# Performance work log

Hardware: AMD Instinct MI355X
Metric: run time of the kernel (lower is better)

## Reference

```python
import jax, jax.numpy as jnp
from jax import lax
import numpy as np

D, H, L, B, T = 64, 16, 8, 4096, 128

def _uniform(key, shape, k):
    return jax.random.uniform(key, shape, jnp.float32, -k, k)

def setup_inputs() -> dict:
    key = jax.random.key(0)
    ks = jax.random.split(key, 16)
    kh = 1.0 / np.sqrt(H)
    kl = 1.0 / np.sqrt(L)
    return {
        "x": jax.random.normal(ks[0], (B, T, D), jnp.float32),
        # encoder LSTM (PyTorch gate order i,f,g,o stacked along dim 0)
        "enc_Wih": _uniform(ks[1], (4 * H, D), kh),
        "enc_Whh": _uniform(ks[2], (4 * H, H), kh),
        "enc_bih": _uniform(ks[3], (4 * H,), kh),
        "enc_bhh": _uniform(ks[4], (4 * H,), kh),
        # to_latent / from_latent linears
        "Wl": _uniform(ks[5], (L, H), kh),
        "bl": _uniform(ks[6], (L,), kh),
        "Wf": _uniform(ks[7], (H, L), kl),
        "bf": _uniform(ks[8], (H,), kl),
        # decoder LSTM (input size H)
        "dec_Wih": _uniform(ks[9], (4 * H, H), kh),
        "dec_Whh": _uniform(ks[10], (4 * H, H), kh),
        "dec_bih": _uniform(ks[11], (4 * H,), kh),
        "dec_bhh": _uniform(ks[12], (4 * H,), kh),
        # output linear H -> D
        "Wo": _uniform(ks[13], (D, H), kh),
        "bo": _uniform(ks[14], (D,), kh),
    }

def _lstm(x_tbd, Wih, Whh, bih, bhh):
    # x_tbd: [T, B, in]; returns (all hidden [T, B, H], final hidden [B, H])
    b = bih + bhh
    nbatch = x_tbd.shape[1]
    h0 = jnp.zeros((nbatch, H), x_tbd.dtype)
    c0 = jnp.zeros((nbatch, H), x_tbd.dtype)
    # precompute input projections for all timesteps (one big GEMM)
    xg = jnp.einsum('tbd,gd->tbg', x_tbd, Wih) + b  # [T, B, 4H]
    def step(carry, xg_t):
        h, c = carry
        gates = xg_t + h @ Whh.T
        i, f, g, o = jnp.split(gates, 4, axis=-1)
        c = jax.nn.sigmoid(f) * c + jax.nn.sigmoid(i) * jnp.tanh(g)
        h = jax.nn.sigmoid(o) * jnp.tanh(c)
        return (h, c), h
    (hT, _), hs = lax.scan(step, (h0, c0), xg)
    return hs, hT

def reference(x, enc_Wih, enc_Whh, enc_bih, enc_bhh, Wl, bl, Wf, bf,
              dec_Wih, dec_Whh, dec_bih, dec_bhh, Wo, bo):
    seq = x.shape[1]
    x_t = jnp.swapaxes(x, 0, 1)  # [T, B, D]
    _, h_enc = _lstm(x_t, enc_Wih, enc_Whh, enc_bih, enc_bhh)  # [B, H]
    latent = h_enc @ Wl.T + bl                                  # [B, L]
    rep = latent @ Wf.T + bf                                    # [B, H]
    rep_t = jnp.broadcast_to(rep[None], (seq,) + rep.shape)     # [T, B, H]
    hs, _ = _lstm(rep_t, dec_Wih, dec_Whh, dec_bih, dec_bhh)    # [T, B, H]
    out = jnp.einsum('tbh,dh->tbd', hs, Wo) + bo                # [T, B, D]
    return jnp.swapaxes(out, 0, 1)                              # [B, T, D]
```

## Files before the change

kernel.cpp:

```cpp
#include <hip/hip_runtime.h>
#include <stdint.h>


constexpr int Dm = 64, Tm = 128, TB = 16;

typedef __bf16 bf16x8 __attribute__((ext_vector_type(8)));
typedef float f32x4 __attribute__((ext_vector_type(4)));
typedef unsigned int u32x4 __attribute__((ext_vector_type(4)));

__device__ __forceinline__ uint32_t pk_hi(float a, float b) {
  return (__float_as_uint(b) & 0xFFFF0000u) | (__float_as_uint(a) >> 16);
}
__device__ __forceinline__ float trunc_bf(float a) {
  return __uint_as_float(__float_as_uint(a) & 0xFFFF0000u);
}
__device__ __forceinline__ f32x4 mfma16(bf16x8 a, bf16x8 b, f32x4 c) {
  return __builtin_amdgcn_mfma_f32_16x16x32_bf16(a, b, c, 0, 0, 0);
}

__device__ __forceinline__ float fexp2(float x) {
#if __has_builtin(__builtin_amdgcn_exp2f)
  return __builtin_amdgcn_exp2f(x);
#else
  return exp2f(x);
#endif
}
__device__ __forceinline__ float frcp(float x) {
#if __has_builtin(__builtin_amdgcn_rcpf)
  return __builtin_amdgcn_rcpf(x);
#else
  return 1.0f / x;
#endif
}
__device__ __forceinline__ float tanh_(float x) {
  float xc = fminf(15.0f, fmaxf(-15.0f, x));
  float t = fexp2(2.88539008f * xc);
  return (t - 1.0f) * frcp(t + 1.0f);
}
__device__ __forceinline__ void ldsfence() {
  asm volatile("s_waitcnt lgkmcnt(0)" ::: "memory");
}
__device__ __forceinline__ float dot4(float4 a, float4 b, float acc) {
  return fmaf(a.x, b.x, fmaf(a.y, b.y, fmaf(a.z, b.z, fmaf(a.w, b.w, acc))));
}

__global__ __launch_bounds__(256, 4)
void lstm_ae_kernel(const float* __restrict__ x,
                    const float* __restrict__ eWih, const float* __restrict__ eWhh,
                    const float* __restrict__ eBih, const float* __restrict__ eBhh,
                    const float* __restrict__ Wl,   const float* __restrict__ bl,
                    const float* __restrict__ Wf,   const float* __restrict__ bf,
                    const float* __restrict__ dWih, const float* __restrict__ dWhh,
                    const float* __restrict__ dBih, const float* __restrict__ dBhh,
                    const float* __restrict__ Wo,   const float* __restrict__ bo,
                    float* __restrict__ out)
{
  __shared__ u32x4 s_bfrag[16][64];
  __shared__ float s_xu[4][1280];
  __shared__ float s_h[4][16];
  __shared__ float s_wl[128];
  __shared__ float s_wf[128];

  const int tid = threadIdx.x;
  {
    const int wn = tid >> 6, l = tid & 63;
    const int g = wn * 16 + (l & 15);
#pragma unroll
    for (int c = 0; c < 2; ++c) {
      const float* wp = eWih + g * 64 + c * 32 + ((l >> 4) * 8);
      const float4 wa = *(const float4*)(wp);
      const float4 wb = *(const float4*)(wp + 4);
      u32x4 hd, ld_;
      hd.x = pk_hi(wa.x, wa.y); hd.y = pk_hi(wa.z, wa.w);
      hd.z = pk_hi(wb.x, wb.y); hd.w = pk_hi(wb.z, wb.w);
      const float r0 = wa.x - trunc_bf(wa.x), r1 = wa.y - trunc_bf(wa.y);
      const float r2 = wa.z - trunc_bf(wa.z), r3 = wa.w - trunc_bf(wa.w);
      const float r4 = wb.x - trunc_bf(wb.x), r5 = wb.y - trunc_bf(wb.y);
      const float r6 = wb.z - trunc_bf(wb.z), r7 = wb.w - trunc_bf(wb.w);
      ld_.x = pk_hi(r0, r1); ld_.y = pk_hi(r2, r3);
      ld_.z = pk_hi(r4, r5); ld_.w = pk_hi(r6, r7);
      s_bfrag[(wn * 2 + c) * 2 + 0][l] = hd;
      s_bfrag[(wn * 2 + c) * 2 + 1][l] = ld_;
    }
  }
  if (tid < 128) s_wl[tid] = Wl[tid];
  else s_wf[tid - 128] = Wf[tid - 128];
  __syncthreads();

  const int wave = tid >> 6, lane = tid & 63;
  const int q = lane >> 4, j = lane & 15;
  const int b = blockIdx.x * 4 + wave;
  float* sxw = s_xu[wave];

  const float sAct = (q == 2) ? 2.88539008f : -1.44269504f;
  const float qgF  = (q == 2) ? 1.0f : 0.0f;
  const float cmF  = (q == 2) ? -1.0f : 1.0f;

  const float4* wr = (const float4*)(eWhh + lane * 16);
  float4 w0 = wr[0], w1 = wr[1], w2 = wr[2], w3 = wr[3];

  float bv0 = eBih[0 * 16 + j] + eBhh[0 * 16 + j];
  float bv1 = eBih[1 * 16 + j] + eBhh[1 * 16 + j];
  float bv2 = eBih[2 * 16 + j] + eBhh[2 * 16 + j];
  float bv3 = eBih[3 * 16 + j] + eBhh[3 * 16 + j];

  float4 h0 = {0.f, 0.f, 0.f, 0.f}, h1 = h0, h2 = h0, h3 = h0;
  float cst = 0.0f;
  const float* xb = x + (size_t)b * (Tm * Dm);

  float4 xs0 = *(const float4*)(xb + 0 * 256 + lane * 4);
  float4 xs1 = *(const float4*)(xb + 1 * 256 + lane * 4);
  float4 xs2 = *(const float4*)(xb + 2 * 256 + lane * 4);
  float4 xs3 = *(const float4*)(xb + 3 * 256 + lane * 4);

#pragma unroll 1
  for (int tile = 0; tile < Tm / TB; ++tile) {
    *(float4*)&sxw[(4 * 0 + q) * 68 + j * 4] = xs0;
    *(float4*)&sxw[(4 * 1 + q) * 68 + j * 4] = xs1;
    *(float4*)&sxw[(4 * 2 + q) * 68 + j * 4] = xs2;
    *(float4*)&sxw[(4 * 3 + q) * 68 + j * 4] = xs3;

    if (tile < Tm / TB - 1) {
      const float* xt = xb + (tile + 1) * (TB * Dm);
      xs0 = *(const float4*)(xt + 0 * 256 + lane * 4);
      xs1 = *(const float4*)(xt + 1 * 256 + lane * 4);
      xs2 = *(const float4*)(xt + 2 * 256 + lane * 4);
      xs3 = *(const float4*)(xt + 3 * 256 + lane * 4);
    }
    ldsfence();

    const float4 xa0 = *(const float4*)&sxw[j * 68 +  0 + q * 8];
    const float4 xa1 = *(const float4*)&sxw[j * 68 +  0 + q * 8 + 4];
    const float4 xb0 = *(const float4*)&sxw[j * 68 + 32 + q * 8];
    const float4 xb1 = *(const float4*)&sxw[j * 68 + 32 + q * 8 + 4];
    u32x4 ah0u, al0u, ah1u, al1u;
    ah0u.x = pk_hi(xa0.x, xa0.y); ah0u.y = pk_hi(xa0.z, xa0.w);
    ah0u.z = pk_hi(xa1.x, xa1.y); ah0u.w = pk_hi(xa1.z, xa1.w);
    {
      const float r0 = xa0.x - trunc_bf(xa0.x), r1 = xa0.y - trunc_bf(xa0.y);
      const float r2 = xa0.z - trunc_bf(xa0.z), r3 = xa0.w - trunc_bf(xa0.w);
      const float r4 = xa1.x - trunc_bf(xa1.x), r5 = xa1.y - trunc_bf(xa1.y);
      const float r6 = xa1.z - trunc_bf(xa1.z), r7 = xa1.w - trunc_bf(xa1.w);
      al0u.x = pk_hi(r0, r1); al0u.y = pk_hi(r2, r3);
      al0u.z = pk_hi(r4, r5); al0u.w = pk_hi(r6, r7);
    }
    ah1u.x = pk_hi(xb0.x, xb0.y); ah1u.y = pk_hi(xb0.z, xb0.w);
    ah1u.z = pk_hi(xb1.x, xb1.y); ah1u.w = pk_hi(xb1.z, xb1.w);
    {
      const float r0 = xb0.x - trunc_bf(xb0.x), r1 = xb0.y - trunc_bf(xb0.y);
      const float r2 = xb0.z - trunc_bf(xb0.z), r3 = xb0.w - trunc_bf(xb0.w);
      const float r4 = xb1.x - trunc_bf(xb1.x), r5 = xb1.y - trunc_bf(xb1.y);
      const float r6 = xb1.z - trunc_bf(xb1.z), r7 = xb1.w - trunc_bf(xb1.w);
      al1u.x = pk_hi(r0, r1); al1u.y = pk_hi(r2, r3);
      al1u.z = pk_hi(r4, r5); al1u.w = pk_hi(r6, r7);
    }
    const bf16x8 Ah0 = __builtin_bit_cast(bf16x8, ah0u);
    const bf16x8 Al0 = __builtin_bit_cast(bf16x8, al0u);
    const bf16x8 Ah1 = __builtin_bit_cast(bf16x8, ah1u);
    const bf16x8 Al1 = __builtin_bit_cast(bf16x8, al1u);
    ldsfence();

#pragma unroll
    for (int n = 0; n < 4; ++n) {
      const u32x4 bh0u = *(const u32x4*)&s_bfrag[(n * 2 + 0) * 2 + 0][lane];
      const u32x4 bl0u = *(const u32x4*)&s_bfrag[(n * 2 + 0) * 2 + 1][lane];
      const u32x4 bh1u = *(const u32x4*)&s_bfrag[(n * 2 + 1) * 2 + 0][lane];
      const u32x4 bl1u = *(const u32x4*)&s_bfrag[(n * 2 + 1) * 2 + 1][lane];
      const bf16x8 Bh0 = __builtin_bit_cast(bf16x8, bh0u);
      const bf16x8 Bl0 = __builtin_bit_cast(bf16x8, bl0u);
      const bf16x8 Bh1 = __builtin_bit_cast(bf16x8, bh1u);
      const bf16x8 Bl1 = __builtin_bit_cast(bf16x8, bl1u);
      const float bvn = (n == 0) ? bv0 : (n == 1) ? bv1 : (n == 2) ? bv2 : bv3;
      f32x4 a0 = {bvn, bvn, bvn, bvn};
      f32x4 a1 = {0.f, 0.f, 0.f, 0.f};
      a0 = mfma16(Al0, Bh0, a0);
      a1 = mfma16(Al1, Bh1, a1);
      a0 = mfma16(Ah0, Bl0, a0);
      a1 = mfma16(Ah1, Bl1, a1);
      a0 = mfma16(Ah0, Bh0, a0);
      a1 = mfma16(Ah1, Bh1, a1);
      const f32x4 acc = a0 + a1;
      *(f32x4*)&sxw[(n * 16 + j) * 20 + 4 * q] = acc;
    }
    ldsfence();

    float4 xgv = {0.f, 0.f, 0.f, 0.f};
#pragma unroll
    for (int tt = 0; tt < TB; ++tt) {
      if ((tt & 3) == 0) xgv = *(const float4*)&sxw[lane * 20 + tt];
      const float a_in = ((tt & 3) == 0) ? xgv.x : ((tt & 3) == 1) ? xgv.y
                       : ((tt & 3) == 2) ? xgv.z : xgv.w;
      float e0 = dot4(h0, w0, a_in);
      float e1 = dot4(h1, w1, 0.0f);
      e0 = dot4(h2, w2, e0);
      e1 = dot4(h3, w3, e1);
      const float gp = e0 + e1;
      const float xc = fminf(15.0f, fmaxf(-15.0f, gp));
      const float t_ = fexp2(sAct * xc);
      const float av = fmaf(qgF, t_, cmF) * frcp(t_ + 1.0f);
      const float iv = __shfl(av, j);
      const float fv = __shfl(av, 16 + j);
      const float gv = __shfl(av, 32 + j);
      const float ov = __shfl(av, 48 + j);
      cst = fmaf(fv, cst, iv * gv);
      const float hv = ov * tanh_(cst);
      if (q == 0) s_h[wave][j] = hv;
      ldsfence();
      h0 = *(const float4*)&s_h[wave][0];
      h1 = *(const float4*)&s_h[wave][4];
      h2 = *(const float4*)&s_h[wave][8];
      h3 = *(const float4*)&s_h[wave][12];
    }
  }

  float lat[8];
#pragma unroll
  for (int l = 0; l < 8; ++l) {
    const float* wl4 = &s_wl[l * 16];
    float a = bl[l];
#pragma unroll
    for (int k = 0; k < 4; ++k) {
      const float4 wv4 = *(const float4*)&wl4[k * 4];
      const float4 hh = (k == 0) ? h0 : (k == 1) ? h1 : (k == 2) ? h2 : h3;
      a = fmaf(hh.x, wv4.x, fmaf(hh.y, wv4.y, fmaf(hh.z, wv4.z, fmaf(hh.w, wv4.w, a))));
    }
    lat[l] = a;
  }
  float rep[16];
#pragma unroll
  for (int k = 0; k < 16; ++k) {
    const float* wf8 = &s_wf[k * 8];
    float a = bf[k];
#pragma unroll
    for (int l = 0; l < 8; ++l) a = fmaf(lat[l], wf8[l], a);
    rep[k] = a;
  }
  const float* dwr = dWih + lane * 16;
  float dxg = dBih[lane] + dBhh[lane];
#pragma unroll
  for (int k = 0; k < 16; ++k) dxg = fmaf(rep[k], dwr[k], dxg);

  wr = (const float4*)(dWhh + lane * 16);
  w0 = wr[0]; w1 = wr[1]; w2 = wr[2]; w3 = wr[3];
  const float4* wor = (const float4*)(Wo + lane * 16);
  const float4 o0 = wor[0], o1 = wor[1], o2 = wor[2], o3 = wor[3];
  const float bog = bo[lane];

  h0 = h1 = h2 = h3 = make_float4(0.f, 0.f, 0.f, 0.f);
  cst = 0.0f;
  float* op = out + (size_t)b * (Tm * Dm) + lane;
#pragma unroll 1
  for (int t = 0; t < Tm; ++t) {
    float e0 = dot4(h0, w0, dxg);
    float e1 = dot4(h1, w1, 0.0f);
    e0 = dot4(h2, w2, e0);
    e1 = dot4(h3, w3, e1);
    const float gp = e0 + e1;
    const float xc = fminf(15.0f, fmaxf(-15.0f, gp));
    const float t_ = fexp2(sAct * xc);
    const float av = fmaf(qgF, t_, cmF) * frcp(t_ + 1.0f);
    const float iv = __shfl(av, j);
    const float fv = __shfl(av, 16 + j);
    const float gv = __shfl(av, 32 + j);
    const float ov = __shfl(av, 48 + j);
    float p0 = dot4(h0, o0, bog);
    float p1 = dot4(h1, o1, 0.0f);
    p0 = dot4(h2, o2, p0);
    p1 = dot4(h3, o3, p1);
    if (t) op[(t - 1) * 64] = p0 + p1;
    cst = fmaf(fv, cst, iv * gv);
    const float hv = ov * tanh_(cst);
    if (q == 0) s_h[wave][j] = hv;
    ldsfence();
    h0 = *(const float4*)&s_h[wave][0];
    h1 = *(const float4*)&s_h[wave][4];
    h2 = *(const float4*)&s_h[wave][8];
    h3 = *(const float4*)&s_h[wave][12];
  }
  float p0 = dot4(h0, o0, bog);
  float p1 = dot4(h1, o1, 0.0f);
  p0 = dot4(h2, o2, p0);
  p1 = dot4(h3, o3, p1);
  op[(Tm - 1) * 64] = p0 + p1;
}

extern "C" void kernel_launch(void* const* d_in, const int* in_sizes, int n_in,
                              void* d_out, int out_size, void* d_ws, size_t ws_size,
                              hipStream_t stream) {
  const float* x    = (const float*)d_in[0];
  const float* eWih = (const float*)d_in[1];
  const float* eWhh = (const float*)d_in[2];
  const float* eBih = (const float*)d_in[3];
  const float* eBhh = (const float*)d_in[4];
  const float* Wl   = (const float*)d_in[5];
  const float* bl   = (const float*)d_in[6];
  const float* Wf   = (const float*)d_in[7];
  const float* bf   = (const float*)d_in[8];
  const float* dWih = (const float*)d_in[9];
  const float* dWhh = (const float*)d_in[10];
  const float* dBih = (const float*)d_in[11];
  const float* dBhh = (const float*)d_in[12];
  const float* Wo   = (const float*)d_in[13];
  const float* bo   = (const float*)d_in[14];

  dim3 grid(1024), block(256);
  hipLaunchKernelGGL(lstm_ae_kernel, grid, block, 0, stream,
                     x, eWih, eWhh, eBih, eBhh, Wl, bl, Wf, bf,
                     dWih, dWhh, dBih, dBhh, Wo, bo, (float*)d_out);
}
```

Before: 131.4 us.

## Batch decoder output projection per 16-step tile via split-bf16 MFMA

The decoder now keeps each 16-step tile of hidden states in a per-wave LDS history buffer. After the tile it computes the Wo output projection with split-precision bf16 MFMAs (hi/lo three-pass), replacing the per-timestep scalar dot products inside the recurrence. This takes the output GEMV off the serial critical path and writes outputs in tile batches. The sigmoid and tanh formulas are also simplified to a single fma after the reciprocal, and the xg scratch padding shrinks from 20 to 16. The trade-off is extra registers for the Wo fragments, and the split-bf16 path carries a small precision risk.

After: 132.9 us. Within noise of the previous version (+1.2%).

```diff
diff --git a/kernel.cpp b/kernel.cpp
--- a/kernel.cpp
+++ b/kernel.cpp
@@ -16,6 +16,16 @@
 }
 __device__ __forceinline__ f32x4 mfma16(bf16x8 a, bf16x8 b, f32x4 c) {
   return __builtin_amdgcn_mfma_f32_16x16x32_bf16(a, b, c, 0, 0, 0);
+}
+__device__ __forceinline__ void split8(float4 a, float4 b, u32x4& hi, u32x4& lo) {
+  hi.x = pk_hi(a.x, a.y); hi.y = pk_hi(a.z, a.w);
+  hi.z = pk_hi(b.x, b.y); hi.w = pk_hi(b.z, b.w);
+  const float r0 = a.x - trunc_bf(a.x), r1 = a.y - trunc_bf(a.y);
+  const float r2 = a.z - trunc_bf(a.z), r3 = a.w - trunc_bf(a.w);
+  const float r4 = b.x - trunc_bf(b.x), r5 = b.y - trunc_bf(b.y);
+  const float r6 = b.z - trunc_bf(b.z), r7 = b.w - trunc_bf(b.w);
+  lo.x = pk_hi(r0, r1); lo.y = pk_hi(r2, r3);
+  lo.z = pk_hi(r4, r5); lo.w = pk_hi(r6, r7);
 }
 
 __device__ __forceinline__ float fexp2(float x) {
@@ -35,7 +45,7 @@
 __device__ __forceinline__ float tanh_(float x) {
   float xc = fminf(15.0f, fmaxf(-15.0f, x));
   float t = fexp2(2.88539008f * xc);
-  return (t - 1.0f) * frcp(t + 1.0f);
+  return fmaf(-2.0f, frcp(t + 1.0f), 1.0f);
 }
 __device__ __forceinline__ void ldsfence() {
   asm volatile("s_waitcnt lgkmcnt(0)" ::: "memory");
@@ -56,8 +66,8 @@
                     float* __restrict__ out)
 {
   __shared__ u32x4 s_bfrag[16][64];
-  __shared__ float s_xu[4][1280];
-  __shared__ float s_h[4][16];
+  __shared__ float s_xu[4][1088];
+  __shared__ float s_hist[4][256];
   __shared__ float s_wl[128];
   __shared__ float s_wf[128];
 
@@ -68,17 +78,8 @@
 #pragma unroll
     for (int c = 0; c < 2; ++c) {
       const float* wp = eWih + g * 64 + c * 32 + ((l >> 4) * 8);
-      const float4 wa = *(const float4*)(wp);
-      const float4 wb = *(const float4*)(wp + 4);
       u32x4 hd, ld_;
-      hd.x = pk_hi(wa.x, wa.y); hd.y = pk_hi(wa.z, wa.w);
-      hd.z = pk_hi(wb.x, wb.y); hd.w = pk_hi(wb.z, wb.w);
-      const float r0 = wa.x - trunc_bf(wa.x), r1 = wa.y - trunc_bf(wa.y);
-      const float r2 = wa.z - trunc_bf(wa.z), r3 = wa.w - trunc_bf(wa.w);
-      const float r4 = wb.x - trunc_bf(wb.x), r5 = wb.y - trunc_bf(wb.y);
-      const float r6 = wb.z - trunc_bf(wb.z), r7 = wb.w - trunc_bf(wb.w);
-      ld_.x = pk_hi(r0, r1); ld_.y = pk_hi(r2, r3);
-      ld_.z = pk_hi(r4, r5); ld_.w = pk_hi(r6, r7);
+      split8(*(const float4*)(wp), *(const float4*)(wp + 4), hd, ld_);
       s_bfrag[(wn * 2 + c) * 2 + 0][l] = hd;
       s_bfrag[(wn * 2 + c) * 2 + 1][l] = ld_;
     }
@@ -90,11 +91,12 @@
   const int wave = tid >> 6, lane = tid & 63;
   const int q = lane >> 4, j = lane & 15;
   const int b = blockIdx.x * 4 + wave;
-  float* sxw = s_xu[wave];
+  float* sxw  = s_xu[wave];
+  float* hist = s_hist[wave];
 
   const float sAct = (q == 2) ? 2.88539008f : -1.44269504f;
-  const float qgF  = (q == 2) ? 1.0f : 0.0f;
-  const float cmF  = (q == 2) ? -1.0f : 1.0f;
+  const float qgm  = (q == 2) ? -2.0f : 1.0f;
+  const float qga  = (q == 2) ? 1.0f : 0.0f;
 
   const float4* wr = (const float4*)(eWhh + lane * 16);
   float4 w0 = wr[0], w1 = wr[1], w2 = wr[2], w3 = wr[3];
@@ -103,6 +105,23 @@
   float bv1 = eBih[1 * 16 + j] + eBhh[1 * 16 + j];
   float bv2 = eBih[2 * 16 + j] + eBhh[2 * 16 + j];
   float bv3 = eBih[3 * 16 + j] + eBhh[3 * 16 + j];
+
+  bf16x8 WoBh[4], WoBl[4];
+  const float mA = (q < 2) ? 1.0f : 0.0f;
+#pragma unroll
+  for (int n = 0; n < 4; ++n) {
+    const float* wp = Wo + (n * 16 + j) * 16 + (q & 1) * 8;
+    float4 wa = *(const float4*)(wp);
+    float4 wb = *(const float4*)(wp + 4);
+    wa.x *= mA; wa.y *= mA; wa.z *= mA; wa.w *= mA;
+    wb.x *= mA; wb.y *= mA; wb.z *= mA; wb.w *= mA;
+    u32x4 hd, ld_;
+    split8(wa, wb, hd, ld_);
+    WoBh[n] = __builtin_bit_cast(bf16x8, hd);
+    WoBl[n] = __builtin_bit_cast(bf16x8, ld_);
+  }
+  const float bo0 = bo[0 * 16 + j], bo1 = bo[1 * 16 + j];
+  const float bo2 = bo[2 * 16 + j], bo3 = bo[3 * 16 + j];
 
   float4 h0 = {0.f, 0.f, 0.f, 0.f}, h1 = h0, h2 = h0, h3 = h0;
   float cst = 0.0f;
@@ -129,31 +148,11 @@
     }
     ldsfence();
 
-    const float4 xa0 = *(const float4*)&sxw[j * 68 +  0 + q * 8];
-    const float4 xa1 = *(const float4*)&sxw[j * 68 +  0 + q * 8 + 4];
-    const float4 xb0 = *(const float4*)&sxw[j * 68 + 32 + q * 8];
-    const float4 xb1 = *(const float4*)&sxw[j * 68 + 32 + q * 8 + 4];
     u32x4 ah0u, al0u, ah1u, al1u;
-    ah0u.x = pk_hi(xa0.x, xa0.y); ah0u.y = pk_hi(xa0.z, xa0.w);
-    ah0u.z = pk_hi(xa1.x, xa1.y); ah0u.w = pk_hi(xa1.z, xa1.w);
-    {
-      const float r0 = xa0.x - trunc_bf(xa0.x), r1 = xa0.y - trunc_bf(xa0.y);
-      const float r2 = xa0.z - trunc_bf(xa0.z), r3 = xa0.w - trunc_bf(xa0.w);
-      const float r4 = xa1.x - trunc_bf(xa1.x), r5 = xa1.y - trunc_bf(xa1.y);
-      const float r6 = xa1.z - trunc_bf(xa1.z), r7 = xa1.w - trunc_bf(xa1.w);
-      al0u.x = pk_hi(r0, r1); al0u.y = pk_hi(r2, r3);
-      al0u.z = pk_hi(r4, r5); al0u.w = pk_hi(r6, r7);
-    }
-    ah1u.x = pk_hi(xb0.x, xb0.y); ah1u.y = pk_hi(xb0.z, xb0.w);
-    ah1u.z = pk_hi(xb1.x, xb1.y); ah1u.w = pk_hi(xb1.z, xb1.w);
-    {
-      const float r0 = xb0.x - trunc_bf(xb0.x), r1 = xb0.y - trunc_bf(xb0.y);
-      const float r2 = xb0.z - trunc_bf(xb0.z), r3 = xb0.w - trunc_bf(xb0.w);
-      const float r4 = xb1.x - trunc_bf(xb1.x), r5 = xb1.y - trunc_bf(xb1.y);
-      const float r6 = xb1.z - trunc_bf(xb1.z), r7 = xb1.w - trunc_bf(xb1.w);
-      al1u.x = pk_hi(r0, r1); al1u.y = pk_hi(r2, r3);
-      al1u.z = pk_hi(r4, r5); al1u.w = pk_hi(r6, r7);
-    }
+    split8(*(const float4*)&sxw[j * 68 + 0 + q * 8],
+           *(const float4*)&sxw[j * 68 + 0 + q * 8 + 4], ah0u, al0u);
+    split8(*(const float4*)&sxw[j * 68 + 32 + q * 8],
+           *(const float4*)&sxw[j * 68 + 32 + q * 8 + 4], ah1u, al1u);
     const bf16x8 Ah0 = __builtin_bit_cast(bf16x8, ah0u);
     const bf16x8 Al0 = __builtin_bit_cast(bf16x8, al0u);
     const bf16x8 Ah1 = __builtin_bit_cast(bf16x8, ah1u);
@@ -162,32 +161,25 @@
 
 #pragma unroll
     for (int n = 0; n < 4; ++n) {
-      const u32x4 bh0u = *(const u32x4*)&s_bfrag[(n * 2 + 0) * 2 + 0][lane];
-      const u32x4 bl0u = *(const u32x4*)&s_bfrag[(n * 2 + 0) * 2 + 1][lane];
-      const u32x4 bh1u = *(const u32x4*)&s_bfrag[(n * 2 + 1) * 2 + 0][lane];
-      const u32x4 bl1u = *(const u32x4*)&s_bfrag[(n * 2 + 1) * 2 + 1][lane];
-      const bf16x8 Bh0 = __builtin_bit_cast(bf16x8, bh0u);
-      const bf16x8 Bl0 = __builtin_bit_cast(bf16x8, bl0u);
-      const bf16x8 Bh1 = __builtin_bit_cast(bf16x8, bh1u);
-      const bf16x8 Bl1 = __builtin_bit_cast(bf16x8, bl1u);
+      const bf16x8 Bh0 = __builtin_bit_cast(bf16x8, s_bfrag[(n * 2 + 0) * 2 + 0][lane]);
+      const bf16x8 Bl0 = __builtin_bit_cast(bf16x8, s_bfrag[(n * 2 + 0) * 2 + 1][lane]);
+      const bf16x8 Bh1 = __builtin_bit_cast(bf16x8, s_bfrag[(n * 2 + 1) * 2 + 0][lane]);
+      const bf16x8 Bl1 = __builtin_bit_cast(bf16x8, s_bfrag[(n * 2 + 1) * 2 + 1][lane]);
       const float bvn = (n == 0) ? bv0 : (n == 1) ? bv1 : (n == 2) ? bv2 : bv3;
       f32x4 a0 = {bvn, bvn, bvn, bvn};
       f32x4 a1 = {0.f, 0.f, 0.f, 0.f};
-      a0 = mfma16(Al0, Bh0, a0);
-      a1 = mfma16(Al1, Bh1, a1);
-      a0 = mfma16(Ah0, Bl0, a0);
-      a1 = mfma16(Ah1, Bl1, a1);
-      a0 = mfma16(Ah0, Bh0, a0);
-      a1 = mfma16(Ah1, Bh1, a1);
+      a0 = mfma16(Al0, Bh0, a0);  a1 = mfma16(Al1, Bh1, a1);
+      a0 = mfma16(Ah0, Bl0, a0);  a1 = mfma16(Ah1, Bl1, a1);
+      a0 = mfma16(Ah0, Bh0, a0);  a1 = mfma16(Ah1, Bh1, a1);
       const f32x4 acc = a0 + a1;
-      *(f32x4*)&sxw[(n * 16 + j) * 20 + 4 * q] = acc;
+      *(f32x4*)&sxw[(n * 16 + j) * 16 + 4 * q] = acc;
     }
     ldsfence();
 
     float4 xgv = {0.f, 0.f, 0.f, 0.f};
 #pragma unroll
     for (int tt = 0; tt < TB; ++tt) {
-      if ((tt & 3) == 0) xgv = *(const float4*)&sxw[lane * 20 + tt];
+      if ((tt & 3) == 0) xgv = *(const float4*)&sxw[lane * 16 + tt];
       const float a_in = ((tt & 3) == 0) ? xgv.x : ((tt & 3) == 1) ? xgv.y
                        : ((tt & 3) == 2) ? xgv.z : xgv.w;
       float e0 = dot4(h0, w0, a_in);
@@ -197,19 +189,19 @@
       const float gp = e0 + e1;
       const float xc = fminf(15.0f, fmaxf(-15.0f, gp));
       const float t_ = fexp2(sAct * xc);
-      const float av = fmaf(qgF, t_, cmF) * frcp(t_ + 1.0f);
+      const float av = fmaf(qgm, frcp(t_ + 1.0f), qga);
       const float iv = __shfl(av, j);
       const float fv = __shfl(av, 16 + j);
       const float gv = __shfl(av, 32 + j);
       const float ov = __shfl(av, 48 + j);
       cst = fmaf(fv, cst, iv * gv);
       const float hv = ov * tanh_(cst);
-      if (q == 0) s_h[wave][j] = hv;
+      if (q == 0) hist[j] = hv;
       ldsfence();
-      h0 = *(const float4*)&s_h[wave][0];
-      h1 = *(const float4*)&s_h[wave][4];
-      h2 = *(const float4*)&s_h[wave][8];
-      h3 = *(const float4*)&s_h[wave][12];
+      h0 = *(const float4*)&hist[0];
+      h1 = *(const float4*)&hist[4];
+      h2 = *(const float4*)&hist[8];
+      h3 = *(const float4*)&hist[12];
     }
   }
 
@@ -242,46 +234,58 @@
 
   wr = (const float4*)(dWhh + lane * 16);
   w0 = wr[0]; w1 = wr[1]; w2 = wr[2]; w3 = wr[3];
-  const float4* wor = (const float4*)(Wo + lane * 16);
-  const float4 o0 = wor[0], o1 = wor[1], o2 = wor[2], o3 = wor[3];
-  const float bog = bo[lane];
 
   h0 = h1 = h2 = h3 = make_float4(0.f, 0.f, 0.f, 0.f);
   cst = 0.0f;
-  float* op = out + (size_t)b * (Tm * Dm) + lane;
+  float* ob = out + (size_t)b * (Tm * Dm);
 #pragma unroll 1
-  for (int t = 0; t < Tm; ++t) {
-    float e0 = dot4(h0, w0, dxg);
-    float e1 = dot4(h1, w1, 0.0f);
-    e0 = dot4(h2, w2, e0);
-    e1 = dot4(h3, w3, e1);
-    const float gp = e0 + e1;
-    const float xc = fminf(15.0f, fmaxf(-15.0f, gp));
-    const float t_ = fexp2(sAct * xc);
-    const float av = fmaf(qgF, t_, cmF) * frcp(t_ + 1.0f);
-    const float iv = __shfl(av, j);
-    const float fv = __shfl(av, 16 + j);
-    const float gv = __shfl(av, 32 + j);
-    const float ov = __shfl(av, 48 + j);
-    float p0 = dot4(h0, o0, bog);
-    float p1 = dot4(h1, o1, 0.0f);
-    p0 = dot4(h2, o2, p0);
-    p1 = dot4(h3, o3, p1);
-    if (t) op[(t - 1) * 64] = p0 + p1;
-    cst = fmaf(fv, cst, iv * gv);
-    const float hv = ov * tanh_(cst);
-    if (q == 0) s_h[wave][j] = hv;
-    ldsfence();
-    h0 = *(const float4*)&s_h[wave][0];
-    h1 = *(const float4*)&s_h[wave][4];
-    h2 = *(const float4*)&s_h[wave][8];
-    h3 = *(const float4*)&s_h[wave][12];
-  }
-  float p0 = dot4(h0, o0, bog);
-  float p1 = dot4(h1, o1, 0.0f);
-  p0 = dot4(h2, o2, p0);
-  p1 = dot4(h3, o3, p1);
-  op[(Tm - 1) * 64] = p0 + p1;
+  for (int tile = 0; tile < Tm / TB; ++tile) {
+#pragma unroll
+    for (int tt = 0; tt < TB; ++tt) {
+      float e0 = dot4(h0, w0, dxg);
+      float e1 = dot4(h1, w1, 0.0f);
+      e0 = dot4(h2, w2, e0);
+      e1 = dot4(h3, w3, e1);
+      const float gp = e0 + e1;
+      const float xc = fminf(15.0f, fmaxf(-15.0f, gp));
+      const float t_ = fexp2(sAct * xc);
+      const float av = fmaf(qgm, frcp(t_ + 1.0f), qga);
+      const float iv = __shfl(av, j);
+      const float fv = __shfl(av, 16 + j);
+      const float gv = __shfl(av, 32 + j);
+      const float ov = __shfl(av, 48 + j);
+      cst = fmaf(fv, cst, iv * gv);
+      const float hv = ov * tanh_(cst);
+      if (q == 0) hist[tt * 16 + j] = hv;
+      ldsfence();
+      h0 = *(const float4*)&hist[tt * 16 + 0];
+      h1 = *(const float4*)&hist[tt * 16 + 4];
+      h2 = *(const float4*)&hist[tt * 16 + 8];
+      h3 = *(const float4*)&hist[tt * 16 + 12];
+    }
+
+    float4 ha = *(const float4*)&hist[j * 16 + (q & 1) * 8];
+    float4 hb = *(const float4*)&hist[j * 16 + (q & 1) * 8 + 4];
+    ha.x *= mA; ha.y *= mA; ha.z *= mA; ha.w *= mA;
+    hb.x *= mA; hb.y *= mA; hb.z *= mA; hb.w *= mA;
+    u32x4 ahu, alu;
+    split8(ha, hb, ahu, alu);
+    const bf16x8 Ah = __builtin_bit_cast(bf16x8, ahu);
+    const bf16x8 Al = __builtin_bit_cast(bf16x8, alu);
+    float* obt = ob + (size_t)tile * (TB * Dm);
+#pragma unroll
+    for (int n = 0; n < 4; ++n) {
+      const float bon = (n == 0) ? bo0 : (n == 1) ? bo1 : (n == 2) ? bo2 : bo3;
+      f32x4 c0 = {bon, bon, bon, bon};
+      c0 = mfma16(Al, WoBh[n], c0);
+      c0 = mfma16(Ah, WoBl[n], c0);
+      c0 = mfma16(Ah, WoBh[n], c0);
+      obt[(q * 4 + 0) * 64 + n * 16 + j] = c0.x;
+      obt[(q * 4 + 1) * 64 + n * 16 + j] = c0.y;
+      obt[(q * 4 + 2) * 64 + n * 16 + j] = c0.z;
+      obt[(q * 4 + 3) * 64 + n * 16 + j] = c0.w;
+    }
+  }
 }
 
 extern "C" void kernel_launch(void* const* d_in, const int* in_sizes, int n_in,
```
